# Kernel tuning notes

Hardware: AMD Instinct MI355X
Metric: run time of the kernel (lower is better)

The kernel has to match this reference:

```python
import jax, jax.numpy as jnp
import numpy as np

N = 100_000      # nodes
E = 1_600_000    # directed edges (before self-loops)
F_IN = 256       # input node features
H = 128          # hidden_dim
HEADS = 2
C_HEAD = H // HEADS  # 64, GATConv out_channels per head
G = 128          # graphs in batch
NCLS = 10
NEG_SLOPE = 0.2  # PyG GATConv default


def setup_inputs() -> dict:
    key = jax.random.key(0)
    ks = jax.random.split(key, 20)
    p = lambda k, shape: (jax.random.normal(k, shape, jnp.float32) * 0.05)
    x = jax.random.normal(ks[0], (N, F_IN), jnp.float32)
    edge_index = jax.random.randint(ks[1], (2, E), 0, N, dtype=jnp.int64)
    batch = jnp.sort(jax.random.randint(ks[2], (N,), 0, G, dtype=jnp.int64))
    return dict(
        x=x, edge_index=edge_index, batch=batch,
        pre_w=p(ks[3], (F_IN, H)), pre_b=p(ks[4], (H,)),
        w1=p(ks[5], (H, H)), asrc1=p(ks[6], (HEADS, C_HEAD)), adst1=p(ks[7], (HEADS, C_HEAD)), b1=p(ks[8], (H,)),
        w2=p(ks[9], (H, H)), asrc2=p(ks[10], (HEADS, C_HEAD)), adst2=p(ks[11], (HEADS, C_HEAD)), b2=p(ks[12], (H,)),
        post_w1=p(ks[13], (H, H)), post_b1=p(ks[14], (H,)),
        post_w2=p(ks[15], (H, NCLS)), post_b2=p(ks[16], (NCLS,)),
    )


def _gat_conv(h_in, w, a_src, a_dst, b, src, dst):
    # h: [N, heads, c]
    h = (h_in @ w).reshape(N, HEADS, C_HEAD)
    alpha_src = jnp.sum(h * a_src, axis=-1)  # [N, heads]
    alpha_dst = jnp.sum(h * a_dst, axis=-1)  # [N, heads]
    e = jax.nn.leaky_relu(alpha_src[src] + alpha_dst[dst], NEG_SLOPE)  # [E+N, heads]
    # numerically stable softmax over incoming edges of each destination node
    m = jax.ops.segment_max(e, dst, num_segments=N)
    ex = jnp.exp(e - m[dst])
    denom = jax.ops.segment_sum(ex, dst, num_segments=N)
    alpha = ex / denom[dst]                                           # [E+N, heads]
    out = jax.ops.segment_sum(h[src] * alpha[:, :, None], dst, num_segments=N)
    return out.reshape(N, H) + b  # concat heads + bias


def reference(x, edge_index, batch, pre_w, pre_b,
              w1, asrc1, adst1, b1, w2, asrc2, adst2, b2,
              post_w1, post_b1, post_w2, post_b2):
    # PyG GATConv default add_self_loops=True
    loop = jnp.arange(N, dtype=edge_index.dtype)
    src = jnp.concatenate([edge_index[0], loop])
    dst = jnp.concatenate([edge_index[1], loop])

    h = jax.nn.relu(x @ pre_w + pre_b)
    reprs = jax.ops.segment_sum(h, batch, num_segments=G)
    h = jax.nn.relu(_gat_conv(h, w1, asrc1, adst1, b1, src, dst))
    reprs = reprs + jax.ops.segment_sum(h, batch, num_segments=G)
    h = jax.nn.relu(_gat_conv(h, w2, asrc2, adst2, b2, src, dst))
    reprs = reprs + jax.ops.segment_sum(h, batch, num_segments=G)
    z = jax.nn.relu(reprs @ post_w1 + post_b1) @ post_w2 + post_b2
    return jax.nn.log_softmax(z, axis=-1)
```

## Files before the change

### kernel.cpp

```cpp
#include <hip/hip_runtime.h>
#include <hip/hip_bf16.h>
#include <math.h>

#define NNODES 100000
#define NEDGES 1600000
#define FIN 256
#define HDIM 128
#define NGRAPH 128
#define NCLS 10
#define NEG 0.2f

#define NBUCK 98
#define EPB 4096
#define EBLK ((NEDGES + EPB - 1) / EPB)

typedef short bf8 __attribute__((ext_vector_type(8)));
typedef float f4 __attribute__((ext_vector_type(4)));
typedef float f2v __attribute__((ext_vector_type(2)));

__device__ __forceinline__ float lrelu(float x) { return x > 0.f ? x : NEG * x; }

__device__ __forceinline__ unsigned short f2bf(float f) {
  union { float f; unsigned int u; } v; v.f = f;
  unsigned int r = v.u + 0x7fffu + ((v.u >> 16) & 1u);
  return (unsigned short)(r >> 16);
}
__device__ __forceinline__ float bf2f(unsigned short u) {
  union { unsigned int u; float f; } v; v.u = ((unsigned int)u) << 16; return v.f;
}
__device__ __forceinline__ float fast_rcp(float x) {
  float r;
  asm("v_rcp_f32 %0, %1" : "=v"(r) : "v"(x));
  return r;
}
__device__ __forceinline__ unsigned cvt_pk_bf16(float lo, float hi) {
  unsigned r;
  asm("v_cvt_pk_bf16_f32 %0, %1, %2" : "=v"(r) : "v"(lo), "v"(hi));
  return r;
}
__device__ __forceinline__ unsigned short pk_fp8(float a, float b) {
  return (unsigned short)__builtin_amdgcn_cvt_pk_fp8_f32(a, b, 0, false);
}
__device__ __forceinline__ f2v pk_unpack_fp8(unsigned p) {
#if __has_builtin(__builtin_amdgcn_cvt_pk_f32_fp8)
  return __builtin_amdgcn_cvt_pk_f32_fp8((int)p, false);
#else
  f2v r;
  r.x = __builtin_amdgcn_cvt_f32_fp8(p, 0);
  r.y = __builtin_amdgcn_cvt_f32_fp8(p, 1);
  return r;
#endif
}
__device__ __forceinline__ void gload16(const void* gp, void* lp) {
  __builtin_amdgcn_global_load_lds(
      (const __attribute__((address_space(1))) void*)gp,
      (__attribute__((address_space(3))) void*)lp, 16, 0, 0);
}

__global__ __launch_bounds__(256) void convert_transpose(const float* __restrict__ w,
                                                         unsigned short* __restrict__ wt,
                                                         int K) {
  int i = blockIdx.x * 256 + threadIdx.x;
  if (i >= K * 128) return;
  int k = i >> 7, n = i & 127;
  wt[n * K + k] = f2bf(w[(size_t)k * 128 + n]);
}

template<int K, int ABF16>
__global__ __launch_bounds__(256) void gemm_gll(const void* __restrict__ Av,
                                                const unsigned short* __restrict__ Bt,
                                                const float* __restrict__ bias,
                                                unsigned short* __restrict__ Cb,
                                                unsigned short* __restrict__ Cp,
                                                const float* __restrict__ a_src,
                                                const float* __restrict__ a_dst,
                                                float* __restrict__ o_as,
                                                float* __restrict__ o_ad,
                                                int M, int dorelu) {
  constexpr int ABUF = ABF16 ? 4096 : 8192;
  constexpr int SPAN = ABUF + 8192;
  __shared__ alignas(16) char lds[2 * SPAN];
  int tid = threadIdx.x;
  int wv = tid >> 6, lane = tid & 63;
  int quad = lane >> 4, m16 = lane & 15;
  int row0 = blockIdx.x * 64;
  int rA = row0 + wv * 16 + m16; if (rA > M - 1) rA = M - 1;
  int nB0 = wv * 16 + m16, nB1 = (4 + wv) * 16 + m16;

  const unsigned short* Ab = (const unsigned short*)Av;
  const float* Af = (const float*)Av;

  auto stage = [&](int buf, int kb) {
    char* base = lds + buf * SPAN;
    if (ABF16) {
      gload16(&Ab[(size_t)rA * K + kb + quad * 8], base + wv * 1024);
    } else {
      gload16(&Af[(size_t)rA * K + kb + quad * 8],     base + wv * 2048);
      gload16(&Af[(size_t)rA * K + kb + quad * 8 + 4], base + wv * 2048 + 1024);
    }
    char* bb = base + ABUF;
    gload16(&Bt[(size_t)nB0 * K + kb + quad * 8], bb + wv * 1024);
    gload16(&Bt[(size_t)nB1 * K + kb + quad * 8], bb + (4 + wv) * 1024);
  };

  f4 acc[8];
#pragma unroll
  for (int b = 0; b < 8; ++b) acc[b] = (f4){0.f, 0.f, 0.f, 0.f};

  stage(0, 0);
  int cur = 0;
#pragma unroll
  for (int kb = 0; kb < K; kb += 32) {
    __syncthreads();
    if (kb + 32 < K) stage(cur ^ 1, kb + 32);
    const char* base = lds + cur * SPAN;
    bf8 af;
    if (ABF16) {
      af = *(const bf8*)(base + wv * 1024 + lane * 16);
    } else {
      float4 x0 = *(const float4*)(base + wv * 2048 + lane * 16);
      float4 x1 = *(const float4*)(base + wv * 2048 + 1024 + lane * 16);
      union { bf8 v; unsigned u[4]; } r;
      r.u[0] = cvt_pk_bf16(x0.x, x0.y); r.u[1] = cvt_pk_bf16(x0.z, x0.w);
      r.u[2] = cvt_pk_bf16(x1.x, x1.y); r.u[3] = cvt_pk_bf16(x1.z, x1.w);
      af = r.v;
    }
    const char* bb = base + ABUF;
#pragma unroll
    for (int tn = 0; tn < 8; ++tn) {
      bf8 bm = *(const bf8*)(bb + tn * 1024 + lane * 16);
      acc[tn] = __builtin_amdgcn_mfma_f32_16x16x32_bf16(af, bm, acc[tn], 0, 0, 0);
    }
    cur ^= 1;
  }

  if (Cp) {
    if (a_src) {
      float aS[8], aD[8];
#pragma unroll
      for (int tn = 0; tn < 4; ++tn) {
        aS[tn]     = a_src[tn * 16 + m16];
        aS[tn + 4] = a_src[64 + tn * 16 + m16];
        aD[tn]     = a_dst[tn * 16 + m16];
        aD[tn + 4] = a_dst[64 + tn * 16 + m16];
      }
#pragma unroll
      for (int r = 0; r < 4; ++r) {
        int row = row0 + wv * 16 + quad * 4 + r;
        float ps0 = 0.f, ps1 = 0.f, pd0 = 0.f, pd1 = 0.f;
#pragma unroll
        for (int tn = 0; tn < 4; ++tn) {
          float v0 = acc[tn][r], v1 = acc[tn + 4][r];
          ps0 = fmaf(v0, aS[tn], ps0);
          ps1 = fmaf(v1, aS[tn + 4], ps1);
          pd0 = fmaf(v0, aD[tn], pd0);
          pd1 = fmaf(v1, aD[tn + 4], pd1);
        }
#pragma unroll
        for (int o = 8; o; o >>= 1) {
          ps0 += __shfl_xor(ps0, o); ps1 += __shfl_xor(ps1, o);
          pd0 += __shfl_xor(pd0, o); pd1 += __shfl_xor(pd1, o);
        }
        if (m16 == 0 && row < M) {
          o_as[2 * row] = ps0; o_as[2 * row + 1] = ps1;
          o_ad[2 * row] = pd0; o_ad[2 * row + 1] = pd1;
        }
      }
    }
#pragma unroll
    for (int tn = 0; tn < 4; ++tn)
#pragma unroll
      for (int r = 0; r < 4; ++r) {
        int row = row0 + wv * 16 + quad * 4 + r;
        if (row < M) {
          Cp[(size_t)row * 64 + tn * 16 + m16] = pk_fp8(acc[tn][r], acc[tn + 4][r]);
        }
      }
  } else {
#pragma unroll
    for (int tn = 0; tn < 8; ++tn) {
      float bv = bias ? bias[tn * 16 + m16] : 0.f;
#pragma unroll
      for (int r = 0; r < 4; ++r) {
        int row = row0 + wv * 16 + quad * 4 + r;
        if (row < M) {
          float v = acc[tn][r] + bv;
          if (dorelu) v = fmaxf(v, 0.f);
          Cb[(size_t)row * 128 + tn * 16 + m16] = f2bf(v);
        }
      }
    }
  }
}

__global__ void find_starts(const int* __restrict__ batch, int* __restrict__ gstart) {
  int g = threadIdx.x;
  if (g > NGRAPH) return;
  if (g == NGRAPH) { gstart[g] = NNODES; return; }
  int lo = 0, hi = NNODES;
  while (lo < hi) { int mid = (lo + hi) >> 1; if (batch[mid] < g) lo = mid + 1; else hi = mid; }
  gstart[g] = lo;
}

__global__ __launch_bounds__(256) void bin_count(const int* __restrict__ edst,
                                                 int* __restrict__ blockHist) {
  __shared__ int hist[NBUCK];
  int t = threadIdx.x, blk = blockIdx.x;
  if (t < NBUCK) hist[t] = 0;
  __syncthreads();
  int e0 = blk * EPB;
#pragma unroll
  for (int it = 0; it < EPB / 256; ++it) {
    int e = e0 + it * 256 + t;
    if (e < NEDGES) atomicAdd(&hist[((unsigned)edst[e]) >> 10], 1);
  }
  __syncthreads();
  if (t < NBUCK) blockHist[blk * NBUCK + t] = hist[t];
}

__global__ __launch_bounds__(512) void colscan(const int* __restrict__ blockHist,
                                               int* __restrict__ blockBaseCol,
                                               int* __restrict__ bucket_total) {
  __shared__ int s[512];
  int b = blockIdx.x, t = threadIdx.x;
  int v = (t < EBLK) ? blockHist[t * NBUCK + b] : 0;
  s[t] = v;
  __syncthreads();
  for (int off = 1; off < 512; off <<= 1) {
    int u = (t >= off) ? s[t - off] : 0;
    __syncthreads();
    s[t] += u;
    __syncthreads();
  }
  if (t < EBLK) blockBaseCol[b * EBLK + t] = s[t] - v;
  if (t == 511) bucket_total[b] = s[511];
}

__global__ __launch_bounds__(128) void bscan(const int* __restrict__ bucket_total,
                                             int* __restrict__ bucket_ptr) {
  __shared__ int s[128];
  int t = threadIdx.x;
  int v = (t < NBUCK) ? bucket_total[t] : 0;
  s[t] = v;
  __syncthreads();
  for (int off = 1; off < 128; off <<= 1) {
    int u = (t >= off) ? s[t - off] : 0;
    __syncthreads();
    s[t] += u;
    __syncthreads();
  }
  if (t < NBUCK) bucket_ptr[t] = s[t] - v;
  if (t == 127) bucket_ptr[NBUCK] = s[127];
}

__global__ __launch_bounds__(512) void bin_place(const int* __restrict__ esrc,
                                                 const int* __restrict__ edst,
                                                 const int* __restrict__ blockBaseCol,
                                                 const int* __restrict__ bucket_ptr,
                                                 unsigned* __restrict__ stagingG) {
  __shared__ int hist[NBUCK + 1], lbase[NBUCK + 1], lcur[NBUCK + 1], cbase[NBUCK];
  __shared__ int tmp[128];
  __shared__ uint2 st[EPB];
  int t = threadIdx.x, blk = blockIdx.x;
  if (t < NBUCK + 1) hist[t] = 0;
  __syncthreads();
  int e0 = blk * EPB;
#pragma unroll
  for (int it = 0; it < EPB / 512; ++it) {
    int e = e0 + it * 512 + t;
    int b = NBUCK;
    if (e < NEDGES) b = ((unsigned)edst[e]) >> 10;
    atomicAdd(&hist[b], 1);
  }
  __syncthreads();
  if (t < 128) tmp[t] = (t < NBUCK + 1) ? hist[t] : 0;
  __syncthreads();
  for (int off = 1; off < 128; off <<= 1) {
    int u = 0;
    if (t < 128 && t >= off) u = tmp[t - off];
    __syncthreads();
    if (t < 128) tmp[t] += u;
    __syncthreads();
  }
  if (t < NBUCK + 1) { int ex = tmp[t] - hist[t]; lbase[t] = ex; lcur[t] = ex; }
  if (t < NBUCK) cbase[t] = bucket_ptr[t] + blockBaseCol[t * EBLK + blk];
  __syncthreads();
#pragma unroll
  for (int it = 0; it < EPB / 512; ++it) {
    int e = e0 + it * 512 + t;
    unsigned s = 0, d = 0xFFFFFFFFu;
    if (e < NEDGES) { s = (unsigned)esrc[e]; d = (unsigned)edst[e]; }
    int b = (d == 0xFFFFFFFFu) ? NBUCK : (int)(d >> 10);
    int slot = atomicAdd(&lcur[b], 1);
    st[slot] = make_uint2(s, d);
  }
  __syncthreads();
  for (int i = t; i < EPB; i += 512) {
    uint2 ed = st[i];
    if (ed.y == 0xFFFFFFFFu) continue;
    int b = (int)(ed.y >> 10);
    stagingG[cbase[b] + (i - lbase[b])] = ((ed.y & 1023u) << 17) | ed.x;
  }
}

__global__ __launch_bounds__(1024) void bucket_csr_fused(const unsigned* __restrict__ stagingG,
                                                         const int* __restrict__ bucket_ptr,
                                                         int* __restrict__ row_ptr,
                                                         int* __restrict__ colv) {
  __shared__ int dl[1024];
  __shared__ int cur[1024];
  int b = blockIdx.x, t = threadIdx.x;
  dl[t] = 0;
  __syncthreads();
  int s0 = bucket_ptr[b], s1 = bucket_ptr[b + 1];
  for (int j = s0 + t; j < s1; j += 1024)
    atomicAdd(&dl[stagingG[j] >> 17], 1);
  __syncthreads();
  int myDeg = dl[t];
  for (int off = 1; off < 1024; off <<= 1) {
    int u = (t >= off) ? dl[t - off] : 0;
    __syncthreads();
    dl[t] += u;
    __syncthreads();
  }
  int rp = s0 + dl[t] - myDeg;
  cur[t] = rp;
  int n = (b << 10) + t;
  if (n < NNODES) row_ptr[n] = rp;
  if (n == NNODES - 1) row_ptr[NNODES] = rp + myDeg;
  __syncthreads();
  for (int j = s0 + t; j < s1; j += 1024) {
    unsigned v = stagingG[j];
    int pos = atomicAdd(&cur[v >> 17], 1);
    colv[pos] = (int)(v & 0x1FFFFu);
  }
}

__global__ __launch_bounds__(256) void aggregate(const unsigned short* __restrict__ hwb,
                                                 const float* __restrict__ a_s,
                                                 const float* __restrict__ a_d,
                                                 const int* __restrict__ row_ptr,
                                                 const int* __restrict__ colv,
                                                 const float* __restrict__ bias,
                                                 unsigned short* __restrict__ out) {
  __shared__ float2 wsh[256];
  int i = (blockIdx.x * 256 + threadIdx.x) >> 6;
  int lane = threadIdx.x & 63;
  if (i >= NNODES) return;
  i = __builtin_amdgcn_readfirstlane(i);
  int wbase = (threadIdx.x >> 6) * 64;

  float ad0 = a_d[2 * i], ad1 = a_d[2 * i + 1];
  int start = row_ptr[i], end = row_ptr[i + 1];
  int deg = end - start;
  float ws0 = __expf(lrelu(a_s[2 * i] + ad0));
  float ws1 = __expf(lrelu(a_s[2 * i + 1] + ad1));

  int sl = 0; float w0l = 0.f, w1l = 0.f;
  if (lane < deg) {
    sl = colv[start + lane];
    float2 av = *reinterpret_cast<const float2*>(&a_s[2 * sl]);
    w0l = __expf(lrelu(av.x + ad0));
    w1l = __expf(lrelu(av.y + ad1));
  }
  wsh[wbase + lane] = make_float2(w0l, w1l);
  float d0 = w0l, d1 = w1l;
  for (int o = 32; o; o >>= 1) { d0 += __shfl_xor(d0, o); d1 += __shfl_xor(d1, o); }
  float den0 = d0 + ws0, den1 = d1 + ws1;

  unsigned ps = hwb[(size_t)i * 64 + lane];
  f2v pv = pk_unpack_fp8(ps);
  float acc0 = ws0 * pv.x, acc1 = ws1 * pv.y;

  int dmin = deg < 64 ? deg : 64;
  int t = 0;
#define GSTEP(T)                                                               \
  {                                                                            \
    int s = __builtin_amdgcn_readlane(sl, (T));                                \
    unsigned q = hwb[(size_t)s * 64 + lane];                                   \
    float2 w = wsh[wbase + (T)];                    \
    f2v xv = pk_unpack_fp8(q);                                                 \
    acc0 = fmaf(w.x, xv.x, acc0);                                              \
    acc1 = fmaf(w.y, xv.y, acc1);                                              \
  }
  for (; t + 8 <= dmin; t += 8) {
    GSTEP(t);     GSTEP(t + 1); GSTEP(t + 2); GSTEP(t + 3);
    GSTEP(t + 4); GSTEP(t + 5); GSTEP(t + 6); GSTEP(t + 7);
  }
  for (; t < dmin; ++t) { GSTEP(t); }
#undef GSTEP

  for (int j = start + 64; j < end; ++j) {
    int s = colv[j];
    float2 av = *reinterpret_cast<const float2*>(&a_s[2 * s]);
    float w0 = __expf(lrelu(av.x + ad0));
    float w1 = __expf(lrelu(av.y + ad1));
    den0 += w0; den1 += w1;
    unsigned q = hwb[(size_t)s * 64 + lane];
    f2v xv = pk_unpack_fp8(q);
    acc0 = fmaf(w0, xv.x, acc0);
    acc1 = fmaf(w1, xv.y, acc1);
  }

  float r0 = fast_rcp(den0), r1 = fast_rcp(den1);
  float o0 = fmaxf(acc0 * r0 + bias[lane], 0.f);
  float o1 = fmaxf(acc1 * r1 + bias[64 + lane], 0.f);
  unsigned pk = cvt_pk_bf16(o0, o1);
  out[(size_t)i * 128 + lane]      = (unsigned short)pk;
  out[(size_t)i * 128 + 64 + lane] = (unsigned short)(pk >> 16);
}

#define SEG_CHUNK 128
__global__ __launch_bounds__(128) void seg_sum_fast(const unsigned short* __restrict__ h,
                                                    const int* __restrict__ batch,
                                                    const int* __restrict__ gstart,
                                                    float* __restrict__ reprs) {
  int n0 = blockIdx.x * SEG_CHUNK;
  if (n0 >= NNODES) return;
  int nend = n0 + SEG_CHUNK; if (nend > NNODES) nend = NNODES;
  int tid = threadIdx.x;
  int r = n0;
  while (r < nend) {
    int g = batch[r];
    int segend = gstart[g + 1]; if (segend > nend) segend = nend;
    float a0 = 0.f, a1 = 0.f, a2 = 0.f, a3 = 0.f;
    for (; r + 3 < segend; r += 4) {
      a0 += bf2f(h[(size_t)r * 128 + tid]);
      a1 += bf2f(h[(size_t)(r + 1) * 128 + tid]);
      a2 += bf2f(h[(size_t)(r + 2) * 128 + tid]);
      a3 += bf2f(h[(size_t)(r + 3) * 128 + tid]);
    }
    for (; r < segend; ++r) a0 += bf2f(h[(size_t)r * 128 + tid]);
    atomicAdd(&reprs[g * 128 + tid], (a0 + a1) + (a2 + a3));
  }
}

__global__ __launch_bounds__(128) void head_kernel(const float* __restrict__ reprs,
                                                   const float* __restrict__ pw1,
                                                   const float* __restrict__ pb1,
                                                   const float* __restrict__ pw2,
                                                   const float* __restrict__ pb2,
                                                   float* __restrict__ out) {
  __shared__ float r[128], t1[128], z[NCLS];
  int g = blockIdx.x, tid = threadIdx.x;
  r[tid] = reprs[g * 128 + tid];
  __syncthreads();
  float acc = pb1[tid];
  for (int k = 0; k < 128; ++k) acc = fmaf(r[k], pw1[k * 128 + tid], acc);
  t1[tid] = fmaxf(acc, 0.f);
  __syncthreads();
  if (tid < NCLS) {
    float zz = pb2[tid];
    for (int k = 0; k < 128; ++k) zz = fmaf(t1[k], pw2[k * NCLS + tid], zz);
    z[tid] = zz;
  }
  __syncthreads();
  if (tid == 0) {
    float mx = -1e30f;
    for (int c = 0; c < NCLS; ++c) mx = fmaxf(mx, z[c]);
    float s = 0.f;
    for (int c = 0; c < NCLS; ++c) s += expf(z[c] - mx);
    float ls = logf(s) + mx;
    for (int c = 0; c < NCLS; ++c) out[g * NCLS + c] = z[c] - ls;
  }
}

extern "C" void kernel_launch(void* const* d_in, const int* in_sizes, int n_in,
                              void* d_out, int out_size, void* d_ws, size_t ws_size,
                              hipStream_t stream) {
  const float* x     = (const float*)d_in[0];
  const int*   eidx  = (const int*)d_in[1];
  const int*   batch = (const int*)d_in[2];
  const float* pre_w = (const float*)d_in[3];
  const float* pre_b = (const float*)d_in[4];
  const float* w1    = (const float*)d_in[5];
  const float* asrc1 = (const float*)d_in[6];
  const float* adst1 = (const float*)d_in[7];
  const float* b1    = (const float*)d_in[8];
  const float* w2    = (const float*)d_in[9];
  const float* asrc2 = (const float*)d_in[10];
  const float* adst2 = (const float*)d_in[11];
  const float* b2    = (const float*)d_in[12];
  const float* pw1   = (const float*)d_in[13];
  const float* pb1   = (const float*)d_in[14];
  const float* pw2   = (const float*)d_in[15];
  const float* pb2   = (const float*)d_in[16];
  float* out = (float*)d_out;

  const int* esrc = eidx;
  const int* edst = eidx + NEDGES;

  char* wsp = (char*)d_ws;
  size_t off = 0;
  auto alloc = [&](size_t bytes) -> void* {
    void* p = wsp + off;
    off += (bytes + 255) & ~(size_t)255;
    return p;
  };
  unsigned short* hb  = (unsigned short*)alloc((size_t)NNODES * 128 * 2);
  unsigned short* hwb = (unsigned short*)alloc((size_t)NNODES * 64 * 2);
  float* a_s         = (float*)alloc((size_t)NNODES * 2 * 4);
  float* a_d         = (float*)alloc((size_t)NNODES * 2 * 4);
  float* reprs       = (float*)alloc((size_t)NGRAPH * 128 * 4);
  int* gstart        = (int*)alloc((NGRAPH + 1) * 4);
  int* row_ptr       = (int*)alloc(((size_t)NNODES + 1) * 4);
  int* colv          = (int*)alloc((size_t)NEDGES * 4);
  unsigned short* wt_pre = (unsigned short*)alloc((size_t)128 * FIN * 2);
  unsigned short* wt1    = (unsigned short*)alloc((size_t)128 * HDIM * 2);
  unsigned short* wt2    = (unsigned short*)alloc((size_t)128 * HDIM * 2);
  int* blockHist     = (int*)alloc((size_t)EBLK * NBUCK * 4);
  int* blockBaseCol  = (int*)alloc((size_t)NBUCK * EBLK * 4);
  int* bucket_total  = (int*)alloc(NBUCK * 4);
  int* bucket_ptr    = (int*)alloc((NBUCK + 1) * 4);
  unsigned* stagingG = (unsigned*)alloc((size_t)NEDGES * 4);

  int wb = NNODES / 4;
  int sb = (NNODES + SEG_CHUNK - 1) / SEG_CHUNK;
  int gb = (NNODES + 63) / 64;

  convert_transpose<<<(FIN * 128 + 255) / 256, 256, 0, stream>>>(pre_w, wt_pre, FIN);
  convert_transpose<<<(HDIM * 128 + 255) / 256, 256, 0, stream>>>(w1, wt1, HDIM);
  convert_transpose<<<(HDIM * 128 + 255) / 256, 256, 0, stream>>>(w2, wt2, HDIM);

  hipMemsetAsync(reprs, 0, (size_t)NGRAPH * 128 * 4, stream);
  find_starts<<<1, 256, 0, stream>>>(batch, gstart);

  bin_count<<<EBLK, 256, 0, stream>>>(edst, blockHist);
  colscan<<<NBUCK, 512, 0, stream>>>(blockHist, blockBaseCol, bucket_total);
  bscan<<<1, 128, 0, stream>>>(bucket_total, bucket_ptr);
  bin_place<<<EBLK, 512, 0, stream>>>(esrc, edst, blockBaseCol, bucket_ptr, stagingG);
  bucket_csr_fused<<<NBUCK, 1024, 0, stream>>>(stagingG, bucket_ptr, row_ptr, colv);

  gemm_gll<FIN, 0><<<gb, 256, 0, stream>>>(x, wt_pre, pre_b, hb, nullptr,
                                           nullptr, nullptr, nullptr, nullptr, NNODES, 1);
  seg_sum_fast<<<sb, 128, 0, stream>>>(hb, batch, gstart, reprs);

  gemm_gll<HDIM, 1><<<gb, 256, 0, stream>>>(hb, wt1, nullptr, nullptr, hwb,
                                            asrc1, adst1, a_s, a_d, NNODES, 0);
  aggregate<<<wb, 256, 0, stream>>>(hwb, a_s, a_d, row_ptr, colv, b1, hb);
  seg_sum_fast<<<sb, 128, 0, stream>>>(hb, batch, gstart, reprs);

  gemm_gll<HDIM, 1><<<gb, 256, 0, stream>>>(hb, wt2, nullptr, nullptr, hwb,
                                            asrc2, adst2, a_s, a_d, NNODES, 0);
  aggregate<<<wb, 256, 0, stream>>>(hwb, a_s, a_d, row_ptr, colv, b2, hb);
  seg_sum_fast<<<sb, 128, 0, stream>>>(hb, batch, gstart, reprs);

  head_kernel<<<NGRAPH, 128, 0, stream>>>(reprs, pw1, pb1, pw2, pb2, out);
}
```

Before: 467.8 us.

## Fuse per-graph readout into GEMM/aggregate epilogues and restage GEMM B tile

Removes the separate seg_sum kernels and the find_starts kernel. The readout sum is now done with per-element global float atomicAdds into reprs, issued directly from the pre-projection GEMM epilogue and from the aggregate kernel. The GEMM is restructured so B is staged into LDS once per 128-wide K chunk, while each wave loads its own A slices with direct-to-LDS loads and waits on them with explicit vmcnt counters instead of a block barrier every K step. This saves extra passes over the hidden features and some kernel launches. In exchange it issues millions of uncombined atomics onto only 128x128 addresses, and because nodes are sorted by graph, neighbouring threads hit the same addresses and contend heavily.

```diff
diff --git a/kernel.cpp b/kernel.cpp
--- a/kernel.cpp
+++ b/kernel.cpp
@@ -56,6 +56,11 @@
       (const __attribute__((address_space(1))) void*)gp,
       (__attribute__((address_space(3))) void*)lp, 16, 0, 0);
 }
+template<int N>
+__device__ __forceinline__ void vwait() {
+  asm volatile("s_waitcnt vmcnt(%0)" :: "i"(N) : "memory");
+  __builtin_amdgcn_sched_barrier(0);
+}
 
 __global__ __launch_bounds__(256) void convert_transpose(const float* __restrict__ w,
                                                          unsigned short* __restrict__ wt,
@@ -67,72 +72,92 @@
 }
 
 template<int K, int ABF16>
-__global__ __launch_bounds__(256) void gemm_gll(const void* __restrict__ Av,
-                                                const unsigned short* __restrict__ Bt,
-                                                const float* __restrict__ bias,
-                                                unsigned short* __restrict__ Cb,
-                                                unsigned short* __restrict__ Cp,
-                                                const float* __restrict__ a_src,
-                                                const float* __restrict__ a_dst,
-                                                float* __restrict__ o_as,
-                                                float* __restrict__ o_ad,
-                                                int M, int dorelu) {
-  constexpr int ABUF = ABF16 ? 4096 : 8192;
-  constexpr int SPAN = ABUF + 8192;
-  __shared__ alignas(16) char lds[2 * SPAN];
+__global__ __launch_bounds__(256) void gemm_pipe(const void* __restrict__ Av,
+                                                 const unsigned short* __restrict__ Bt,
+                                                 const float* __restrict__ bias,
+                                                 unsigned short* __restrict__ Cb,
+                                                 unsigned short* __restrict__ Cp,
+                                                 const float* __restrict__ a_src,
+                                                 const float* __restrict__ a_dst,
+                                                 float* __restrict__ o_as,
+                                                 float* __restrict__ o_ad,
+                                                 const int* __restrict__ batch,
+                                                 float* __restrict__ reprs,
+                                                 int M, int dorelu) {
+  constexpr int NCH = K / 128;
+  constexpr int L = ABF16 ? 1 : 2;
+  constexpr int ASLOT = ABF16 ? 1024 : 2048;
+  constexpr int BSZ = 32768;
+  __shared__ alignas(16) char lds[BSZ + 16 * ASLOT];
   int tid = threadIdx.x;
   int wv = tid >> 6, lane = tid & 63;
   int quad = lane >> 4, m16 = lane & 15;
   int row0 = blockIdx.x * 64;
   int rA = row0 + wv * 16 + m16; if (rA > M - 1) rA = M - 1;
-  int nB0 = wv * 16 + m16, nB1 = (4 + wv) * 16 + m16;
 
   const unsigned short* Ab = (const unsigned short*)Av;
   const float* Af = (const float*)Av;
 
-  auto stage = [&](int buf, int kb) {
-    char* base = lds + buf * SPAN;
+  auto stageBs = [&](int ch) {
+#pragma unroll
+    for (int i2 = 0; i2 < 8; ++i2) {
+      int j = i2 * 256 + tid;
+      int l = j & 63, tn = (j >> 6) & 7, ktl = j >> 9;
+      int n = tn * 16 + (l & 15);
+      int k = ch * 128 + ktl * 32 + (l >> 4) * 8;
+      *(bf8*)(lds + j * 16) = *(const bf8*)&Bt[(size_t)n * K + k];
+    }
+  };
+  auto stageA = [&](int kt, int s) {
+    char* rb = lds + BSZ + (wv * 4 + s) * ASLOT;
+    int kb = kt * 32;
     if (ABF16) {
-      gload16(&Ab[(size_t)rA * K + kb + quad * 8], base + wv * 1024);
+      gload16(&Ab[(size_t)rA * K + kb + quad * 8], rb);
     } else {
-      gload16(&Af[(size_t)rA * K + kb + quad * 8],     base + wv * 2048);
-      gload16(&Af[(size_t)rA * K + kb + quad * 8 + 4], base + wv * 2048 + 1024);
+      gload16(&Af[(size_t)rA * K + kb + quad * 8],     rb);
+      gload16(&Af[(size_t)rA * K + kb + quad * 8 + 4], rb + 1024);
     }
-    char* bb = base + ABUF;
-    gload16(&Bt[(size_t)nB0 * K + kb + quad * 8], bb + wv * 1024);
-    gload16(&Bt[(size_t)nB1 * K + kb + quad * 8], bb + (4 + wv) * 1024);
   };
 
   f4 acc[8];
 #pragma unroll
   for (int b = 0; b < 8; ++b) acc[b] = (f4){0.f, 0.f, 0.f, 0.f};
 
-  stage(0, 0);
-  int cur = 0;
-#pragma unroll
-  for (int kb = 0; kb < K; kb += 32) {
-    __syncthreads();
-    if (kb + 32 < K) stage(cur ^ 1, kb + 32);
-    const char* base = lds + cur * SPAN;
-    bf8 af;
-    if (ABF16) {
-      af = *(const bf8*)(base + wv * 1024 + lane * 16);
-    } else {
-      float4 x0 = *(const float4*)(base + wv * 2048 + lane * 16);
-      float4 x1 = *(const float4*)(base + wv * 2048 + 1024 + lane * 16);
-      union { bf8 v; unsigned u[4]; } r;
-      r.u[0] = cvt_pk_bf16(x0.x, x0.y); r.u[1] = cvt_pk_bf16(x0.z, x0.w);
-      r.u[2] = cvt_pk_bf16(x1.x, x1.y); r.u[3] = cvt_pk_bf16(x1.z, x1.w);
-      af = r.v;
-    }
-    const char* bb = base + ABUF;
-#pragma unroll
-    for (int tn = 0; tn < 8; ++tn) {
-      bf8 bm = *(const bf8*)(bb + tn * 1024 + lane * 16);
-      acc[tn] = __builtin_amdgcn_mfma_f32_16x16x32_bf16(af, bm, acc[tn], 0, 0, 0);
-    }
-    cur ^= 1;
-  }
+#define CONS(S, NW)                                                            \
+  {                                                                            \
+    vwait<NW>();                                                               \
+    const char* rb = lds + BSZ + (wv * 4 + (S)) * ASLOT;                       \
+    bf8 af;                                                                    \
+    if (ABF16) {                                                               \
+      af = *(const bf8*)(rb + lane * 16);                                      \
+    } else {                                                                   \
+      float4 x0 = *(const float4*)(rb + lane * 16);                            \
+      float4 x1 = *(const float4*)(rb + 1024 + lane * 16);                     \
+      union { bf8 v; unsigned u[4]; } rr;                                      \
+      rr.u[0] = cvt_pk_bf16(x0.x, x0.y); rr.u[1] = cvt_pk_bf16(x0.z, x0.w);    \
+      rr.u[2] = cvt_pk_bf16(x1.x, x1.y); rr.u[3] = cvt_pk_bf16(x1.z, x1.w);    \
+      af = rr.v;                                                               \
+    }                                                                          \
+    _Pragma("unroll")                                                          \
+    for (int tn = 0; tn < 8; ++tn) {                                           \
+      bf8 bm = *(const bf8*)(lds + ((S) * 512 + tn * 64 + lane) * 16);         \
+      acc[tn] = __builtin_amdgcn_mfma_f32_16x16x32_bf16(af, bm, acc[tn], 0, 0, 0); \
+    }                                                                          \
+  }
+
+  stageBs(0);
+  __syncthreads();
+#pragma unroll
+  for (int ch = 0; ch < NCH; ++ch) {
+    if (ch) { __syncthreads(); stageBs(ch); __syncthreads(); }
+#pragma unroll
+    for (int s = 0; s < 4; ++s) stageA(ch * 4 + s, s);
+    CONS(0, 3 * L);
+    CONS(1, 2 * L);
+    CONS(2, 1 * L);
+    CONS(3, 0);
+  }
+#undef CONS
 
   if (Cp) {
     if (a_src) {
@@ -177,6 +202,12 @@
         }
       }
   } else {
+    int bR[4];
+#pragma unroll
+    for (int r = 0; r < 4; ++r) {
+      int row = row0 + wv * 16 + quad * 4 + r;
+      bR[r] = (row < M) ? batch[row] : 0;
+    }
 #pragma unroll
     for (int tn = 0; tn < 8; ++tn) {
       float bv = bias ? bias[tn * 16 + m16] : 0.f;
@@ -187,19 +218,11 @@
           float v = acc[tn][r] + bv;
           if (dorelu) v = fmaxf(v, 0.f);
           Cb[(size_t)row * 128 + tn * 16 + m16] = f2bf(v);
+          atomicAdd(&reprs[bR[r] * 128 + tn * 16 + m16], v);
         }
       }
     }
   }
-}
-
-__global__ void find_starts(const int* __restrict__ batch, int* __restrict__ gstart) {
-  int g = threadIdx.x;
-  if (g > NGRAPH) return;
-  if (g == NGRAPH) { gstart[g] = NNODES; return; }
-  int lo = 0, hi = NNODES;
-  while (lo < hi) { int mid = (lo + hi) >> 1; if (batch[mid] < g) lo = mid + 1; else hi = mid; }
-  gstart[g] = lo;
 }
 
 __global__ __launch_bounds__(256) void bin_count(const int* __restrict__ edst,
@@ -342,6 +365,8 @@
                                                  const int* __restrict__ row_ptr,
                                                  const int* __restrict__ colv,
                                                  const float* __restrict__ bias,
+                                                 const int* __restrict__ batch,
+                                                 float* __restrict__ reprs,
                                                  unsigned short* __restrict__ out) {
   __shared__ float2 wsh[256];
   int i = (blockIdx.x * 256 + threadIdx.x) >> 6;
@@ -408,31 +433,9 @@
   unsigned pk = cvt_pk_bf16(o0, o1);
   out[(size_t)i * 128 + lane]      = (unsigned short)pk;
   out[(size_t)i * 128 + 64 + lane] = (unsigned short)(pk >> 16);
-}
-
-#define SEG_CHUNK 128
-__global__ __launch_bounds__(128) void seg_sum_fast(const unsigned short* __restrict__ h,
-                                                    const int* __restrict__ batch,
-                                                    const int* __restrict__ gstart,
-                                                    float* __restrict__ reprs) {
-  int n0 = blockIdx.x * SEG_CHUNK;
-  if (n0 >= NNODES) return;
-  int nend = n0 + SEG_CHUNK; if (nend > NNODES) nend = NNODES;
-  int tid = threadIdx.x;
-  int r = n0;
-  while (r < nend) {
-    int g = batch[r];
-    int segend = gstart[g + 1]; if (segend > nend) segend = nend;
-    float a0 = 0.f, a1 = 0.f, a2 = 0.f, a3 = 0.f;
-    for (; r + 3 < segend; r += 4) {
-      a0 += bf2f(h[(size_t)r * 128 + tid]);
-      a1 += bf2f(h[(size_t)(r + 1) * 128 + tid]);
-      a2 += bf2f(h[(size_t)(r + 2) * 128 + tid]);
-      a3 += bf2f(h[(size_t)(r + 3) * 128 + tid]);
-    }
-    for (; r < segend; ++r) a0 += bf2f(h[(size_t)r * 128 + tid]);
-    atomicAdd(&reprs[g * 128 + tid], (a0 + a1) + (a2 + a3));
-  }
+  int g = batch[i];
+  atomicAdd(&reprs[g * 128 + lane], o0);
+  atomicAdd(&reprs[g * 128 + 64 + lane], o1);
 }
 
 __global__ __launch_bounds__(128) void head_kernel(const float* __restrict__ reprs,
@@ -502,7 +505,6 @@
   float* a_s         = (float*)alloc((size_t)NNODES * 2 * 4);
   float* a_d         = (float*)alloc((size_t)NNODES * 2 * 4);
   float* reprs       = (float*)alloc((size_t)NGRAPH * 128 * 4);
-  int* gstart        = (int*)alloc((NGRAPH + 1) * 4);
   int* row_ptr       = (int*)alloc(((size_t)NNODES + 1) * 4);
   int* colv          = (int*)alloc((size_t)NEDGES * 4);
   unsigned short* wt_pre = (unsigned short*)alloc((size_t)128 * FIN * 2);
@@ -515,7 +517,6 @@
   unsigned* stagingG = (unsigned*)alloc((size_t)NEDGES * 4);
 
   int wb = NNODES / 4;
-  int sb = (NNODES + SEG_CHUNK - 1) / SEG_CHUNK;
   int gb = (NNODES + 63) / 64;
 
   convert_transpose<<<(FIN * 128 + 255) / 256, 256, 0, stream>>>(pre_w, wt_pre, FIN);
@@ -523,7 +524,6 @@
   convert_transpose<<<(HDIM * 128 + 255) / 256, 256, 0, stream>>>(w2, wt2, HDIM);
 
   hipMemsetAsync(reprs, 0, (size_t)NGRAPH * 128 * 4, stream);
-  find_starts<<<1, 256, 0, stream>>>(batch, gstart);
 
   bin_count<<<EBLK, 256, 0, stream>>>(edst, blockHist);
   colscan<<<NBUCK, 512, 0, stream>>>(blockHist, blockBaseCol, bucket_total);
@@ -531,19 +531,19 @@
   bin_place<<<EBLK, 512, 0, stream>>>(esrc, edst, blockBaseCol, bucket_ptr, stagingG);
   bucket_csr_fused<<<NBUCK, 1024, 0, stream>>>(stagingG, bucket_ptr, row_ptr, colv);
 
-  gemm_gll<FIN, 0><<<gb, 256, 0, stream>>>(x, wt_pre, pre_b, hb, nullptr,
-                                           nullptr, nullptr, nullptr, nullptr, NNODES, 1);
-  seg_sum_fast<<<sb, 128, 0, stream>>>(hb, batch, gstart, reprs);
-
-  gemm_gll<HDIM, 1><<<gb, 256, 0, stream>>>(hb, wt1, nullptr, nullptr, hwb,
-                                            asrc1, adst1, a_s, a_d, NNODES, 0);
-  aggregate<<<wb, 256, 0, stream>>>(hwb, a_s, a_d, row_ptr, colv, b1, hb);
-  seg_sum_fast<<<sb, 128, 0, stream>>>(hb, batch, gstart, reprs);
-
-  gemm_gll<HDIM, 1><<<gb, 256, 0, stream>>>(hb, wt2, nullptr, nullptr, hwb,
-                                            asrc2, adst2, a_s, a_d, NNODES, 0);
-  aggregate<<<wb, 256, 0, stream>>>(hwb, a_s, a_d, row_ptr, colv, b2, hb);
-  seg_sum_fast<<<sb, 128, 0, stream>>>(hb, batch, gstart, reprs);
+  gemm_pipe<FIN, 0><<<gb, 256, 0, stream>>>(x, wt_pre, pre_b, hb, nullptr,
+                                            nullptr, nullptr, nullptr, nullptr,
+                                            batch, reprs, NNODES, 1);
+
+  gemm_pipe<HDIM, 1><<<gb, 256, 0, stream>>>(hb, wt1, nullptr, nullptr, hwb,
+                                             asrc1, adst1, a_s, a_d,
+                                             nullptr, nullptr, NNODES, 0);
+  aggregate<<<wb, 256, 0, stream>>>(hwb, a_s, a_d, row_ptr, colv, b1, batch, reprs, hb);
+
+  gemm_pipe<HDIM, 1><<<gb, 256, 0, stream>>>(hb, wt2, nullptr, nullptr, hwb,
+                                             asrc2, adst2, a_s, a_d,
+                                             nullptr, nullptr, NNODES, 0);
+  aggregate<<<wb, 256, 0, stream>>>(hwb, a_s, a_d, row_ptr, colv, b2, batch, reprs, hb);
 
   head_kernel<<<NGRAPH, 128, 0, stream>>>(reprs, pw1, pb1, pw2, pb2, out);
 }
```

Result: slower. 888.7 us (+90.0%).
